# Kernel tuning notes

Measured on AMD Instinct MI355X. Metric: run time of the kernel, lower is better.

Reference implementation:

```python
import jax, jax.numpy as jnp
import numpy as np


def _layernorm(x, g, b, eps=1e-5):
    mu = jnp.mean(x, axis=-1, keepdims=True)
    var = jnp.var(x, axis=-1, keepdims=True)
    return (x - mu) * jax.lax.rsqrt(var + eps) * g + b


def _forward(x_real, x_imag, dt, conv_w, conv_b, spec_re, spec_im, lam_re, lam_im,
             dt_param, sigma, noise_r, noise_i, ln_g, ln_b, W1, b1, w2, b2,
             Jg_W, Jg_b, Rg_W, Rg_b):
    B, T, C, H, W = x_real.shape
    x = x_real + 1j * x_imag  # complex field [B,T,C,H,W]

    # ---- spatial mixer: 3x3 conv applied to real/imag parts (linear op) ----
    def conv(z):
        z2 = z.reshape(B * T, C, H, W)
        y = jax.lax.conv_general_dilated(z2, conv_w, (1, 1), 'SAME',
                                         dimension_numbers=('NCHW', 'OIHW', 'NCHW'))
        return (y + conv_b[None, :, None, None]).reshape(B, T, C, H, W)
    x = x + (conv(x.real) + 1j * conv(x.imag))

    # ---- spectral mixer: pointwise complex filter in FFT domain ----
    Xf = jnp.fft.fft2(x, axes=(-2, -1), norm='ortho')
    filt = (spec_re + 1j * spec_im)[None, None]  # [1,1,C,H,W]
    x = x + jnp.fft.ifft2(Xf * filt, axes=(-2, -1), norm='ortho')

    # ---- metriplectic propagator: diagonal SSM scan in rfft2 space ----
    dt_eff = dt * jax.nn.softplus(dt_param)          # [C]
    dt_scalar = dt_eff.mean()
    xs = jnp.concatenate([x.real, x.imag], axis=0)   # [2B,T,C,H,W]; B_out=2B
    u = jnp.fft.rfft2(xs, axes=(-2, -1), norm='ortho')  # [2B,T,C,H,Wf]
    lam = -jax.nn.softplus(lam_re) + 1j * lam_im     # stable poles, [C]
    A = jnp.exp(lam * dt_eff.astype(jnp.complex64))  # [C]
    A = jnp.broadcast_to(A[None, None, :, None, None], u.shape)

    def comb(e1, e2):  # first-order linear recurrence h_t = a_t h_{t-1} + u_t
        a1, u1 = e1
        a2, u2 = e2
        return (a1 * a2, a2 * u1 + u2)
    _, h = jax.lax.associative_scan(comb, (A, u), axis=1)

    xt = jnp.fft.irfft2(h, s=(H, W), axes=(-2, -1), norm='ortho')  # [2B,T,C,H,W] real
    x_temporal = xt[:B] + 1j * xt[B:]

    noise = (noise_r + 1j * noise_i) * sigma * jnp.sqrt(dt_scalar)
    x = x + x_temporal + noise

    # ---- Port-Hamiltonian layer on real||imag channel concat ----
    xp = jnp.transpose(x, (0, 1, 3, 4, 2))                  # [B,T,H,W,C]
    xc = jnp.concatenate([xp.real, xp.imag], axis=-1)       # [B,T,H,W,2C]
    D = 2 * C
    x_in = _layernorm(xc, ln_g, ln_b)
    # grads of potential H = sum(MLP(x_in)) wrt x_in
    pot = lambda z: (jax.nn.silu(z @ W1 + b1) @ w2 + b2).sum()
    grads = jax.grad(pot)(x_in)
    M = (x_in @ Jg_W + Jg_b).reshape(*xc.shape[:-1], D, D)
    Jm = M - jnp.swapaxes(M, -1, -2)
    P = (x_in @ Rg_W + Rg_b).reshape(*xc.shape[:-1], D, D)
    R = jnp.einsum('...ki,...kj->...ij', P, P) + 1e-4 * jnp.eye(D, dtype=xc.dtype)
    update = jnp.einsum('...ij,...j->...i', Jm - R, grads)
    x_ph = xc + update * dt_scalar

    # output: [B,T,2C,H,W]; real half = out.real, imag half = out.imag
    return jnp.transpose(x_ph, (0, 1, 4, 2, 3))


def setup_inputs() -> dict:
    key = jax.random.key(0)
    ks = jax.random.split(key, 16)
    B, T, C, H, W = 2, 8, 16, 64, 64
    D = 2 * C
    hid = D * 4
    f32 = jnp.float32
    rn = lambda k, s, sc=1.0: jax.random.normal(k, s, f32) * sc
    return dict(
        x_real=rn(ks[0], (B, T, C, H, W)),
        x_imag=rn(ks[1], (B, T, C, H, W)),
        dt=jnp.asarray(0.1, f32),
        conv_w=rn(ks[2], (C, C, 3, 3), 0.05),
        conv_b=jnp.zeros((C,), f32),
        spec_re=rn(ks[3], (C, H, W), 0.1),
        spec_im=rn(ks[4], (C, H, W), 0.1),
        lam_re=rn(ks[5], (C,)),
        lam_im=rn(ks[6], (C,)),
        dt_param=rn(ks[7], (C,)),
        sigma=jnp.asarray(0.01, f32),
        noise_r=rn(ks[8], (B, T, C, H, W)),
        noise_i=rn(ks[9], (B, T, C, H, W)),
        ln_g=jnp.ones((D,), f32),
        ln_b=jnp.zeros((D,), f32),
        W1=rn(ks[10], (D, hid), 0.1),
        b1=jnp.zeros((hid,), f32),
        w2=rn(ks[11], (hid,), 0.1),
        b2=jnp.asarray(0.0, f32),
        Jg_W=rn(ks[12], (D, D * D), 0.02),
        Jg_b=jnp.zeros((D * D,), f32),
        Rg_W=rn(ks[13], (D, D * D), 0.02),
        Rg_b=jnp.zeros((D * D,), f32),
    )


def reference(x_real, x_imag, dt, conv_w, conv_b, spec_re, spec_im, lam_re, lam_im,
              dt_param, sigma, noise_r, noise_i, ln_g, ln_b, W1, b1, w2, b2,
              Jg_W, Jg_b, Rg_W, Rg_b):
    return _forward(x_real, x_imag, dt, conv_w, conv_b, spec_re, spec_im, lam_re,
                    lam_im, dt_param, sigma, noise_r, noise_i, ln_g, ln_b, W1, b1,
                    w2, b2, Jg_W, Jg_b, Rg_W, Rg_b)
```

## Files before the change

kernel.cpp:

```cpp
#include <hip/hip_runtime.h>
#include <math.h>

#define Bb 2
#define Tt 8
#define Cc 16
#define Hh 64
#define Ww 64
#define Dd 32
#define HID 128
#define NPIX 4096
#define NIMG 256

typedef unsigned short ushort_t;
typedef unsigned int uint_t;
typedef __attribute__((ext_vector_type(8))) short short8;
typedef __attribute__((ext_vector_type(4))) float f32x4;
union U16 { uint4 u; short8 s; };

__device__ __forceinline__ float sp_f(float x) {
    return (x > 20.f) ? x : log1pf(expf(x));
}

__device__ __forceinline__ ushort_t f2bf(float f) {
    uint_t u = __float_as_uint(f);
    uint_t r = (u + 0x7fffu + ((u >> 16) & 1u)) >> 16;
    return (ushort_t)r;
}
__device__ __forceinline__ float bf2f(ushort_t h) { return __uint_as_float(((uint_t)h) << 16); }

__device__ __forceinline__ uint_t packbf(float hi, float lo) {
    return __builtin_amdgcn_perm(__float_as_uint(hi), __float_as_uint(lo), 0x07060302u);
}
__device__ __forceinline__ uint4 synth8(const float* gf, float xs) {
    uint4 r;
    r.x = packbf(gf[1] * xs, gf[0] * xs);
    r.y = packbf(gf[3] * xs, gf[2] * xs);
    r.z = packbf(gf[5] * xs, gf[4] * xs);
    r.w = packbf(gf[7] * xs, gf[6] * xs);
    return r;
}
__device__ __forceinline__ void expand8(uint4 v, float* f) {
    f[0] = __uint_as_float(v.x << 16); f[1] = __uint_as_float(v.x & 0xffff0000u);
    f[2] = __uint_as_float(v.y << 16); f[3] = __uint_as_float(v.y & 0xffff0000u);
    f[4] = __uint_as_float(v.z << 16); f[5] = __uint_as_float(v.z & 0xffff0000u);
    f[6] = __uint_as_float(v.w << 16); f[7] = __uint_as_float(v.w & 0xffff0000u);
}

typedef __attribute__((address_space(1))) const void cgvoid;
typedef __attribute__((address_space(3))) void svoid;
__device__ __forceinline__ void gload_lds16(const void* g, void* l) {
    __builtin_amdgcn_global_load_lds((cgvoid*)g, (svoid*)l, 16, 0, 0);
}

#define MFMA16(a, b, c) __builtin_amdgcn_mfma_f32_16x16x32_bf16((a), (b), (c), 0, 0, 0)

struct cpx { float r, i; };
__device__ __forceinline__ cpx cadd(cpx a, cpx b) { return {a.r + b.r, a.i + b.i}; }
__device__ __forceinline__ cpx csub(cpx a, cpx b) { return {a.r - b.r, a.i - b.i}; }
__device__ __forceinline__ cpx cmulw(cpx a, float wr, float wi) {
    return {a.r * wr - a.i * wi, a.r * wi + a.i * wr};
}
template<int S>
__device__ __forceinline__ cpx cmulSi(cpx a) {
    return {-(float)S * a.i, (float)S * a.r};
}
template<int S>
__device__ __forceinline__ void dft8(cpx* y) {
    const float C = 0.70710678118654752f;
    cpx t0 = cadd(y[0], y[4]), t1 = csub(y[0], y[4]);
    cpx t2 = cadd(y[2], y[6]), t3 = csub(y[2], y[6]);
    cpx e0 = cadd(t0, t2), e2 = csub(t0, t2);
    cpx t3i = cmulSi<S>(t3);
    cpx e1 = cadd(t1, t3i), e3 = csub(t1, t3i);
    cpx u0 = cadd(y[1], y[5]), u1 = csub(y[1], y[5]);
    cpx u2 = cadd(y[3], y[7]), u3 = csub(y[3], y[7]);
    cpx o0 = cadd(u0, u2), o2 = csub(u0, u2);
    cpx u3i = cmulSi<S>(u3);
    cpx o1 = cadd(u1, u3i), o3 = csub(u1, u3i);
    o1 = cmulw(o1, C, (float)S * C);
    o2 = cmulSi<S>(o2);
    o3 = cmulw(o3, -C, (float)S * C);
    y[0] = cadd(e0, o0); y[4] = csub(e0, o0);
    y[1] = cadd(e1, o1); y[5] = csub(e1, o1);
    y[2] = cadd(e2, o2); y[6] = csub(e2, o2);
    y[3] = cadd(e3, o3); y[7] = csub(e3, o3);
}

template<int S>
__device__ __forceinline__ void fft2d_r8(float* reM, float* imM,
                                         const float* twr, const float* twi, int tid) {
    int j = tid & 63, q = tid >> 6;
    #pragma unroll
    for (int nn = 0; nn < 2; ++nn) {
        int n2 = q * 2 + nn;
        cpx y[8];
        #pragma unroll
        for (int n1 = 0; n1 < 8; ++n1) {
            int a = j * 65 + n1 * 8 + n2;
            y[n1] = {reM[a], imM[a]};
        }
        dft8<S>(y);
        #pragma unroll
        for (int k1 = 0; k1 < 8; ++k1) {
            int m = (n2 * k1) & 63;
            cpx b = cmulw(y[k1], twr[m], twi[m]);
            int a = j * 65 + k1 * 8 + n2;
            reM[a] = b.r; imM[a] = b.i;
        }
    }
    __syncthreads();
    cpx yb[2][8];
    #pragma unroll
    for (int kk = 0; kk < 2; ++kk) {
        int k1 = q * 2 + kk;
        #pragma unroll
        for (int n2 = 0; n2 < 8; ++n2) {
            int a = j * 65 + k1 * 8 + n2;
            yb[kk][n2] = {reM[a], imM[a]};
        }
        dft8<S>(yb[kk]);
    }
    __syncthreads();
    #pragma unroll
    for (int kk = 0; kk < 2; ++kk) {
        int k1 = q * 2 + kk;
        #pragma unroll
        for (int k2 = 0; k2 < 8; ++k2) {
            int a = j * 65 + k1 + k2 * 8;
            reM[a] = yb[kk][k2].r; imM[a] = yb[kk][k2].i;
        }
    }
    __syncthreads();
    #pragma unroll
    for (int nn = 0; nn < 2; ++nn) {
        int n2 = q * 2 + nn;
        cpx y[8];
        #pragma unroll
        for (int n1 = 0; n1 < 8; ++n1) {
            int a = (n1 * 8 + n2) * 65 + j;
            y[n1] = {reM[a], imM[a]};
        }
        dft8<S>(y);
        #pragma unroll
        for (int k1 = 0; k1 < 8; ++k1) {
            int m = (n2 * k1) & 63;
            cpx b = cmulw(y[k1], twr[m], twi[m]);
            int a = (k1 * 8 + n2) * 65 + j;
            reM[a] = b.r; imM[a] = b.i;
        }
    }
    __syncthreads();
    #pragma unroll
    for (int kk = 0; kk < 2; ++kk) {
        int k1 = q * 2 + kk;
        #pragma unroll
        for (int n2 = 0; n2 < 8; ++n2) {
            int a = (k1 * 8 + n2) * 65 + j;
            yb[kk][n2] = {reM[a], imM[a]};
        }
        dft8<S>(yb[kk]);
    }
    __syncthreads();
    #pragma unroll
    for (int kk = 0; kk < 2; ++kk) {
        int k1 = q * 2 + kk;
        #pragma unroll
        for (int k2 = 0; k2 < 8; ++k2) {
            int a = (k1 + k2 * 8) * 65 + j;
            reM[a] = yb[kk][k2].r; imM[a] = yb[kk][k2].i;
        }
    }
    __syncthreads();
}

__global__ __launch_bounds__(256)
void k_conv(const float* __restrict__ xr, const float* __restrict__ xi,
            const float* __restrict__ cw, const float* __restrict__ cb,
            float2* __restrict__ x1,
            const float* __restrict__ JW, const float* __restrict__ Jb,
            const float* __restrict__ RW, const float* __restrict__ Rb,
            const float* __restrict__ W1, const float* __restrict__ dtp,
            const float* __restrict__ dt_param,
            ushort_t* __restrict__ B1t, ushort_t* __restrict__ B2t,
            ushort_t* __restrict__ w1n, ushort_t* __restrict__ w1t,
            float* __restrict__ dts_out) {
    __shared__ float sre[Cc][18][18];
    __shared__ float sim[Cc][18][18];
    __shared__ float swt[8 * 16 * 12];
    __shared__ float sb[8];
    int tid = threadIdx.x;
    if (blockIdx.x >= 512) {
        const int N1 = 96 * 1152, N2 = 32 * 1152, N3 = 4096;
        int i = (blockIdx.x - 512) * 256 + tid;
        for (; i < N1 + N2 + N3; i += 40 * 256) {
            if (i < N1) {
                int n = i / 1152, k = i % 1152;
                float v = 0.f;
                if (k < 1024) {
                    int d = k >> 5, r = k & 31;
                    if (n < 32)      v = JW[d * 1024 + n * 32 + r];
                    else if (n < 64) v = JW[d * 1024 + r * 32 + (n - 32)];
                    else             v = RW[d * 1024 + (n - 64) * 32 + r];
                } else if (k < 1056) {
                    int r = k - 1024;
                    if (n < 32)      v = Jb[n * 32 + r];
                    else if (n < 64) v = Jb[r * 32 + (n - 32)];
                    else             v = Rb[(n - 64) * 32 + r];
                }
                B1t[i] = f2bf(v);
            } else if (i < N1 + N2) {
                int i2 = i - N1;
                int n = i2 / 1152, k = i2 % 1152;
                float v = 0.f;
                if (k < 1024) {
                    int d = k >> 5, kk = k & 31;
                    v = RW[d * 1024 + kk * 32 + n];
                } else if (k < 1056) {
                    v = Rb[(k - 1024) * 32 + n];
                }
                B2t[i2] = f2bf(v);
            } else {
                int i3 = i - N1 - N2;
                int d = i3 >> 7, h = i3 & 127;
                ushort_t v = f2bf(W1[i3]);
                w1n[i3] = v;
                w1t[h * 32 + d] = v;
            }
        }
        if (blockIdx.x == 512 && tid == 0) {
            float s = 0.f;
            for (int c = 0; c < Cc; ++c) s += sp_f(dt_param[c]);
            dts_out[0] = dtp[0] * s * (1.f / Cc);
        }
        return;
    }
    int blk = blockIdx.x;
    int bt = blk >> 5;
    int sub = blk & 31;
    int tile = sub >> 1, cohalf = sub & 1;
    int ty0 = (tile >> 2) * 16, tx0 = (tile & 3) * 16;
    for (int i = tid; i < 8 * 16 * 9; i += 256) {
        int g = i / 9, k = i % 9;
        swt[g * 12 + k] = cw[cohalf * 8 * 144 + i];
    }
    if (tid < 8) sb[tid] = cb[cohalf * 8 + tid];
    for (int i = tid; i < Cc * 18 * 18; i += 256) {
        int ci = i / 324; int r = i % 324; int y = r / 18, x = r % 18;
        int gy = ty0 + y - 1, gx = tx0 + x - 1;
        float vr = 0.f, vi = 0.f;
        if (gy >= 0 && gy < Hh && gx >= 0 && gx < Ww) {
            int gidx = (bt * Cc + ci) * NPIX + gy * Ww + gx;
            vr = xr[gidx]; vi = xi[gidx];
        }
        sre[ci][y][x] = vr; sim[ci][y][x] = vi;
    }
    __syncthreads();
    int py = tid >> 4, px = tid & 15;
    int gy = ty0 + py, gx = tx0 + px;
    float ar[8], ai[8];
    #pragma unroll
    for (int oc = 0; oc < 8; ++oc) {
        int cg = cohalf * 8 + oc;
        ar[oc] = sre[cg][py + 1][px + 1] + sb[oc];
        ai[oc] = sim[cg][py + 1][px + 1] + sb[oc];
    }
    for (int ci = 0; ci < Cc; ++ci) {
        float nr[9], ni[9];
        #pragma unroll
        for (int dy = 0; dy < 3; ++dy)
            #pragma unroll
            for (int dx = 0; dx < 3; ++dx) {
                nr[dy * 3 + dx] = sre[ci][py + dy][px + dx];
                ni[dy * 3 + dx] = sim[ci][py + dy][px + dx];
            }
        #pragma unroll
        for (int oc = 0; oc < 8; ++oc) {
            const float* wp = &swt[(oc * 16 + ci) * 12];
            float4 w0 = *(const float4*)&wp[0];
            float4 w1 = *(const float4*)&wp[4];
            float w8 = wp[8];
            ar[oc] += w0.x * nr[0] + w0.y * nr[1] + w0.z * nr[2]
                    + w0.w * nr[3] + w1.x * nr[4] + w1.y * nr[5]
                    + w1.z * nr[6] + w1.w * nr[7] + w8 * nr[8];
            ai[oc] += w0.x * ni[0] + w0.y * ni[1] + w0.z * ni[2]
                    + w0.w * ni[3] + w1.x * ni[4] + w1.y * ni[5]
                    + w1.z * ni[6] + w1.w * ni[7] + w8 * ni[8];
        }
    }
    #pragma unroll
    for (int oc = 0; oc < 8; ++oc)
        x1[(bt * Cc + cohalf * 8 + oc) * NPIX + gy * Ww + gx] = make_float2(ar[oc], ai[oc]);
}

__global__ __launch_bounds__(256)
void k_fft_fwd(const float2* __restrict__ x1,
               const float* __restrict__ spec_re, const float* __restrict__ spec_im,
               float2* __restrict__ X2f) {
    int img = blockIdx.x;
    int c = img % Cc;
    int tid = threadIdx.x;
    __shared__ float re[64 * 65], im[64 * 65];
    __shared__ float twr[64], twi[64];
    if (tid < 64) {
        float ang = -0.098174770424681038798f * (float)tid;
        twr[tid] = cosf(ang); twi[tid] = sinf(ang);
    }
    const float2* src = x1 + (size_t)img * NPIX;
    for (int idx = tid; idx < NPIX; idx += 256) {
        int h = idx >> 6, w = idx & 63;
        float2 v = src[idx];
        re[h * 65 + w] = v.x; im[h * 65 + w] = v.y;
    }
    __syncthreads();
    fft2d_r8<-1>(re, im, twr, twi, tid);
    const float* fr = spec_re + c * NPIX;
    const float* fi = spec_im + c * NPIX;
    float2* dst = X2f + (size_t)img * NPIX;
    for (int idx = tid; idx < NPIX; idx += 256) {
        int h = idx >> 6, w = idx & 63;
        float xr_ = re[h * 65 + w], xi_ = im[h * 65 + w];
        float gr = 1.f + fr[idx], gi = fi[idx];
        dst[idx] = make_float2(xr_ * gr - xi_ * gi, xi_ * gr + xr_ * gi);
    }
}

__global__ __launch_bounds__(256)
void k_scan2(const float2* __restrict__ Z,
             const float* __restrict__ lam_re, const float* __restrict__ lam_im,
             const float* __restrict__ dt_param, const float* __restrict__ dtp,
             float2* __restrict__ S) {
    int id = blockIdx.x * 256 + threadIdx.x;
    int w = id & 63;
    int c = (id >> 12) & 15;
    int b = id >> 16;
    float dte = dtp[0] * sp_f(dt_param[c]);
    float ea = expf(-sp_f(lam_re[c]) * dte);
    float ph = lam_im[c] * dte;
    float Ar = ea * cosf(ph), Ai = ea * sinf(ph);
    if (w > 32) Ai = -Ai;
    bool sc = (w == 0) || (w == 32);
    int pix = id & (NPIX - 1);
    int base = (b * Tt * Cc + c) * NPIX + pix;
    float s1r = 0.f, s1i = 0.f, s2r = 0.f, s2i = 0.f;
    #pragma unroll
    for (int t = 0; t < Tt; ++t) {
        int idx = base + t * (Cc * NPIX);
        float2 zv = Z[idx];
        float nr = Ar * s1r - Ai * s1i + zv.x;
        float ni = Ar * s1i + Ai * s1r + zv.y;
        s1r = nr; s1i = ni;
        float zr, zi;
        if (sc) {
            nr = Ar * s2r + Ai * s2i + zv.x;
            ni = Ar * s2i - Ai * s2r + zv.y;
            s2r = nr; s2i = ni;
            zr = 0.5f * (s1r + s2r); zi = 0.5f * (s1i + s2i);
        } else { zr = s1r; zi = s1i; }
        S[idx] = make_float2(zv.x + zr, zv.y + zi);
    }
}

__global__ __launch_bounds__(256)
void k_fft_inv(const float2* __restrict__ Sp,
               const float* __restrict__ noise_r, const float* __restrict__ noise_i,
               const float* __restrict__ sigma_p, const float* __restrict__ dts_p,
               float2* __restrict__ xf) {
    int img = blockIdx.x; int tid = threadIdx.x;
    __shared__ float re[64 * 65], im[64 * 65];
    __shared__ float twr[64], twi[64];
    if (tid < 64) {
        float ang = 0.098174770424681038798f * (float)tid;
        twr[tid] = cosf(ang); twi[tid] = sinf(ang);
    }
    const float2* src = Sp + (size_t)img * NPIX;
    for (int idx = tid; idx < NPIX; idx += 256) {
        int h = idx >> 6, w = idx & 63;
        float2 v = src[idx];
        re[h * 65 + w] = v.x; im[h * 65 + w] = v.y;
    }
    __syncthreads();
    fft2d_r8<1>(re, im, twr, twi, tid);
    float ns = sigma_p[0] * sqrtf(dts_p[0]);
    const float inv = 1.f / 4096.f;
    float2* dst = xf + (size_t)img * NPIX;
    const float* nr = noise_r + (size_t)img * NPIX;
    const float* ni = noise_i + (size_t)img * NPIX;
    for (int idx = tid; idx < NPIX; idx += 256) {
        int h = idx >> 6, w = idx & 63;
        dst[idx] = make_float2(re[h * 65 + w] * inv + ns * nr[idx],
                               im[h * 65 + w] * inv + ns * ni[idx]);
    }
}

__global__ __launch_bounds__(256, 2)
void k_ph(const float2* __restrict__ field,
          const float* __restrict__ ln_g, const float* __restrict__ ln_b,
          const float* __restrict__ b1, const float* __restrict__ w2,
          const ushort_t* __restrict__ w1n, const ushort_t* __restrict__ w1t,
          const ushort_t* __restrict__ B1t, const ushort_t* __restrict__ B2t,
          const float* __restrict__ dts_p,
          float* __restrict__ out) {
    __shared__ ushort_t xin_s[128 * 40];
    __shared__ ushort_t g_s[128 * 40];
    __shared__ ushort_t pg_s[128 * 40];
    __shared__ ushort_t A_s[128 * 136];

    int tid = threadIdx.x;
    int bt = blockIdx.x >> 5;
    int pix0 = (blockIdx.x & 31) << 7;

    int p = tid & 127, half = tid >> 7;
    const float2* fbase = field + ((size_t)bt * 16) * NPIX + pix0 + p;
    float2 xv[8];
    float s1 = 0.f, s2 = 0.f;
    #pragma unroll
    for (int j = 0; j < 8; ++j) {
        xv[j] = fbase[(half * 8 + j) * NPIX];
        s1 += xv[j].x + xv[j].y;
        s2 += xv[j].x * xv[j].x + xv[j].y * xv[j].y;
    }
    float2* red = (float2*)A_s;
    red[p * 2 + half] = make_float2(s1, s2);
    __syncthreads();
    float2 r0 = red[p * 2], r1 = red[p * 2 + 1];
    float mu = (r0.x + r1.x) * 0.03125f;
    float var = (r0.y + r1.y) * 0.03125f - mu * mu;
    float rs = rsqrtf(var + 1e-5f);
    #pragma unroll
    for (int j = 0; j < 8; ++j) {
        int cf = half * 8 + j;
        xin_s[p * 40 + cf]      = f2bf((xv[j].x - mu) * rs * ln_g[cf] + ln_b[cf]);
        xin_s[p * 40 + cf + 16] = f2bf((xv[j].y - mu) * rs * ln_g[cf + 16] + ln_b[cf + 16]);
    }
    __syncthreads();

    int lane = tid & 63, wv = tid >> 6;
    int quad = lane >> 4, l15 = lane & 15;
    const f32x4 zero4 = {0.f, 0.f, 0.f, 0.f};

    int m0z = wv * 32;
    f32x4 zacc[2][8];
    #pragma unroll
    for (int mt = 0; mt < 2; ++mt)
        #pragma unroll
        for (int nt = 0; nt < 8; ++nt) zacc[mt][nt] = zero4;
    U16 az[2];
    #pragma unroll
    for (int mt = 0; mt < 2; ++mt)
        az[mt].u = *(const uint4*)&xin_s[(m0z + mt * 16 + l15) * 40 + quad * 8];
    #pragma unroll
    for (int nt = 0; nt < 8; ++nt) {
        U16 bz;
        bz.u = *(const uint4*)&w1t[(nt * 16 + l15) * 32 + quad * 8];
        zacc[0][nt] = MFMA16(az[0].s, bz.s, zacc[0][nt]);
        zacc[1][nt] = MFMA16(az[1].s, bz.s, zacc[1][nt]);
    }
    #pragma unroll
    for (int nt = 0; nt < 8; ++nt) {
        int col = nt * 16 + l15;
        float b1v = b1[col], w2v = w2[col];
        #pragma unroll
        for (int mt = 0; mt < 2; ++mt) {
            #pragma unroll
            for (int r = 0; r < 4; ++r) {
                int row = m0z + mt * 16 + quad * 4 + r;
                float z = zacc[mt][nt][r] + b1v;
                float s = 1.f / (1.f + expf(-z));
                float t = s * (1.f + z * (1.f - s)) * w2v;
                A_s[row * 136 + col] = f2bf(t);
            }
        }
    }

    f32x4 gacc[2][2];
    #pragma unroll
    for (int mt = 0; mt < 2; ++mt)
        #pragma unroll
        for (int nt = 0; nt < 2; ++nt) gacc[mt][nt] = zero4;
    #pragma unroll
    for (int q = 0; q < 4; ++q) {
        U16 ag[2];
        #pragma unroll
        for (int mt = 0; mt < 2; ++mt)
            ag[mt].u = *(const uint4*)&A_s[(m0z + mt * 16 + l15) * 136 + q * 32 + quad * 8];
        #pragma unroll
        for (int nt = 0; nt < 2; ++nt) {
            U16 bg;
            bg.u = *(const uint4*)&w1n[(nt * 16 + l15) * 128 + q * 32 + quad * 8];
            gacc[0][nt] = MFMA16(ag[0].s, bg.s, gacc[0][nt]);
            gacc[1][nt] = MFMA16(ag[1].s, bg.s, gacc[1][nt]);
        }
    }
    #pragma unroll
    for (int mt = 0; mt < 2; ++mt)
        #pragma unroll
        for (int nt = 0; nt < 2; ++nt)
            #pragma unroll
            for (int r = 0; r < 4; ++r)
                g_s[(m0z + mt * 16 + quad * 4 + r) * 40 + nt * 16 + l15] = f2bf(gacc[mt][nt][r]);
    __syncthreads();

    int mh = wv & 1, nh = wv >> 1;
    ushort_t* stage = A_s;
    uint_t xw[4][16];
    uint4 gvp[4];
    float gf[4][8];
    #pragma unroll
    for (int mt = 0; mt < 4; ++mt) {
        int row = mh * 64 + mt * 16 + l15;
        #pragma unroll
        for (int q = 0; q < 4; ++q)
            *(uint4*)&xw[mt][q * 4] = *(const uint4*)&xin_s[row * 40 + q * 8];
        gvp[mt] = *(const uint4*)&g_s[row * 40 + quad * 8];
        expand8(gvp[mt], gf[mt]);
    }

    {
        const ushort_t* gp;
        if (wv == 0) {
            gp = B1t + (0 * 16 + (lane & 15)) * 1152 + (lane >> 4) * 8;
            gload_lds16(gp, stage + 0 * 512);
            gp = B1t + (4 * 16 + (lane & 15)) * 1152 + (lane >> 4) * 8;
            gload_lds16(gp, stage + 4 * 512);
        } else if (wv == 1) {
            gp = B1t + (1 * 16 + (lane & 15)) * 1152 + (lane >> 4) * 8;
            gload_lds16(gp, stage + 1 * 512);
            gp = B1t + (5 * 16 + (lane & 15)) * 1152 + (lane >> 4) * 8;
            gload_lds16(gp, stage + 5 * 512);
        } else if (wv == 2) {
            gp = B1t + (2 * 16 + (lane & 15)) * 1152 + (lane >> 4) * 8;
            gload_lds16(gp, stage + 2 * 512);
        } else {
            gp = B1t + (3 * 16 + (lane & 15)) * 1152 + (lane >> 4) * 8;
            gload_lds16(gp, stage + 3 * 512);
        }
    }
    f32x4 acc1[3][4];
    #pragma unroll
    for (int j = 0; j < 3; ++j)
        #pragma unroll
        for (int mt = 0; mt < 4; ++mt) acc1[j][mt] = zero4;
    #pragma unroll
    for (int s = 0; s < 33; ++s) {
        __syncthreads();
        int par = s & 1;
        if (s < 32) {
            int sn = s + 1, pn = sn & 1;
            const ushort_t* gp;
            if (wv == 0) {
                gp = B1t + (0 * 16 + (lane & 15)) * 1152 + sn * 32 + (lane >> 4) * 8;
                gload_lds16(gp, stage + pn * 3072 + 0 * 512);
                gp = B1t + (4 * 16 + (lane & 15)) * 1152 + sn * 32 + (lane >> 4) * 8;
                gload_lds16(gp, stage + pn * 3072 + 4 * 512);
            } else if (wv == 1) {
                gp = B1t + (1 * 16 + (lane & 15)) * 1152 + sn * 32 + (lane >> 4) * 8;
                gload_lds16(gp, stage + pn * 3072 + 1 * 512);
                gp = B1t + (5 * 16 + (lane & 15)) * 1152 + sn * 32 + (lane >> 4) * 8;
                gload_lds16(gp, stage + pn * 3072 + 5 * 512);
            } else if (wv == 2) {
                gp = B1t + (2 * 16 + (lane & 15)) * 1152 + sn * 32 + (lane >> 4) * 8;
                gload_lds16(gp, stage + pn * 3072 + 2 * 512);
            } else {
                gp = B1t + (3 * 16 + (lane & 15)) * 1152 + sn * 32 + (lane >> 4) * 8;
                gload_lds16(gp, stage + pn * 3072 + 3 * 512);
            }
        }
        U16 bfr[3];
        #pragma unroll
        for (int j = 0; j < 3; ++j)
            bfr[j].u = *(const uint4*)&stage[par * 3072 + (nh + 2 * j) * 512 + lane * 8];
        #pragma unroll
        for (int mt = 0; mt < 4; ++mt) {
            U16 a;
            if (s < 32) {
                uint_t u = xw[mt][s >> 1];
                float xs = (s & 1) ? __uint_as_float(u & 0xffff0000u)
                                   : __uint_as_float(u << 16);
                a.u = synth8(gf[mt], xs);
            } else {
                a.u = gvp[mt];
            }
            #pragma unroll
            for (int j = 0; j < 3; ++j)
                acc1[j][mt] = MFMA16(a.s, bfr[j].s, acc1[j][mt]);
        }
    }
    f32x4 um[4];
    #pragma unroll
    for (int mt = 0; mt < 4; ++mt) {
        um[mt] = acc1[0][mt] - acc1[1][mt];
        #pragma unroll
        for (int r = 0; r < 4; ++r)
            pg_s[(mh * 64 + mt * 16 + quad * 4 + r) * 40 + nh * 16 + l15] = f2bf(acc1[2][mt][r]);
    }
    __syncthreads();

    uint4 pgp[4];
    float pgf[4][8];
    #pragma unroll
    for (int mt = 0; mt < 4; ++mt) {
        int row = mh * 64 + mt * 16 + l15;
        pgp[mt] = *(const uint4*)&pg_s[row * 40 + quad * 8];
        expand8(pgp[mt], pgf[mt]);
    }
    {
        if (wv == 2) {
            const ushort_t* gp = B2t + (0 * 16 + (lane & 15)) * 1152 + (lane >> 4) * 8;
            gload_lds16(gp, stage + 0 * 512);
        } else if (wv == 3) {
            const ushort_t* gp = B2t + (1 * 16 + (lane & 15)) * 1152 + (lane >> 4) * 8;
            gload_lds16(gp, stage + 1 * 512);
        }
    }
    f32x4 acc2[4];
    #pragma unroll
    for (int mt = 0; mt < 4; ++mt) acc2[mt] = zero4;
    #pragma unroll
    for (int s = 0; s < 33; ++s) {
        __syncthreads();
        int par = s & 1;
        if (s < 32) {
            int sn = s + 1, pn = sn & 1;
            if (wv == 2) {
                const ushort_t* gp = B2t + (0 * 16 + (lane & 15)) * 1152 + sn * 32 + (lane >> 4) * 8;
                gload_lds16(gp, stage + pn * 3072 + 0 * 512);
            } else if (wv == 3) {
                const ushort_t* gp = B2t + (1 * 16 + (lane & 15)) * 1152 + sn * 32 + (lane >> 4) * 8;
                gload_lds16(gp, stage + pn * 3072 + 1 * 512);
            }
        }
        U16 bfr;
        bfr.u = *(const uint4*)&stage[par * 3072 + nh * 512 + lane * 8];
        #pragma unroll
        for (int mt = 0; mt < 4; ++mt) {
            U16 a;
            if (s < 32) {
                uint_t u = xw[mt][s >> 1];
                float xs = (s & 1) ? __uint_as_float(u & 0xffff0000u)
                                   : __uint_as_float(u << 16);
                a.u = synth8(pgf[mt], xs);
            } else {
                a.u = pgp[mt];
            }
            acc2[mt] = MFMA16(a.s, bfr.s, acc2[mt]);
        }
    }

    __syncthreads();
    float* upd = (float*)&A_s[8192];
    #pragma unroll
    for (int mt = 0; mt < 4; ++mt) {
        int col = nh * 16 + l15;
        #pragma unroll
        for (int r = 0; r < 4; ++r) {
            int row = mh * 64 + mt * 16 + quad * 4 + r;
            float gval = bf2f(g_s[row * 40 + col]);
            upd[row * 33 + col] = um[mt][r] - acc2[mt][r] - 1e-4f * gval;
        }
    }
    __syncthreads();
    float dts = dts_p[0];
    #pragma unroll
    for (int cc = 0; cc < 16; ++cc) {
        int c = half * 16 + cc;
        float2 v = fbase[cc * NPIX];
        float xcv = half ? v.y : v.x;
        out[((size_t)bt * 32 + c) * NPIX + pix0 + p] = xcv + dts * upd[p * 33 + c];
    }
}

extern "C" void kernel_launch(void* const* d_in, const int* in_sizes, int n_in,
                              void* d_out, int out_size, void* d_ws, size_t ws_size,
                              hipStream_t stream) {
    const float* x_real   = (const float*)d_in[0];
    const float* x_imag   = (const float*)d_in[1];
    const float* dt       = (const float*)d_in[2];
    const float* conv_w   = (const float*)d_in[3];
    const float* conv_b   = (const float*)d_in[4];
    const float* spec_re  = (const float*)d_in[5];
    const float* spec_im  = (const float*)d_in[6];
    const float* lam_re   = (const float*)d_in[7];
    const float* lam_im   = (const float*)d_in[8];
    const float* dt_param = (const float*)d_in[9];
    const float* sigma    = (const float*)d_in[10];
    const float* noise_r  = (const float*)d_in[11];
    const float* noise_i  = (const float*)d_in[12];
    const float* ln_g     = (const float*)d_in[13];
    const float* ln_b     = (const float*)d_in[14];
    const float* W1       = (const float*)d_in[15];
    const float* b1       = (const float*)d_in[16];
    const float* w2       = (const float*)d_in[17];
    const float* Jg_W     = (const float*)d_in[19];
    const float* Jg_b     = (const float*)d_in[20];
    const float* Rg_W     = (const float*)d_in[21];
    const float* Rg_b     = (const float*)d_in[22];

    float2* wsA = (float2*)d_ws;
    float2* wsB = wsA + 1048576;
    float2* wsS = wsB + 1048576;

    ushort_t* B1t = (ushort_t*)(wsS + 1048576);
    ushort_t* B2t = B1t + 96 * 1152;
    ushort_t* w1n = B2t + 32 * 1152;
    ushort_t* w1t = w1n + 4096;
    float*    dts = (float*)(w1t + 4096);

    k_conv<<<552, 256, 0, stream>>>(x_real, x_imag, conv_w, conv_b, wsA,
                                    Jg_W, Jg_b, Rg_W, Rg_b, W1, dt, dt_param,
                                    B1t, B2t, w1n, w1t, dts);
    k_fft_fwd<<<NIMG, 256, 0, stream>>>(wsA, spec_re, spec_im, wsB);
    k_scan2<<<512, 256, 0, stream>>>(wsB, lam_re, lam_im, dt_param, dt, wsS);
    k_fft_inv<<<NIMG, 256, 0, stream>>>(wsS, noise_r, noise_i, sigma, dts, wsA);
    k_ph<<<512, 256, 0, stream>>>(wsA, ln_g, ln_b, b1, w2, w1n, w1t, B1t, B2t, dts,
                                  (float*)d_out);
}
```

Measured before the change: 213.7 us.

## Pre-swizzle PH weights into fragment order and double FFT block threads

The Port-Hamiltonian GEMM weights are now written by the prep kernel directly in per-lane MFMA fragment order. Each wave loads its B fragments straight from global memory into registers with a two-deep prefetch, replacing the LDS staging through global_load_lds and the per-step __syncthreads. Separately, the FFT kernels move from 256 to 512 threads so each thread handles one radix-8 column group instead of two, which lowers register pressure and raises parallelism per image. The trade-off is more redundant global/L2 traffic per wave and higher register use for the prefetched fragments.

```diff
diff --git a/kernel.cpp b/kernel.cpp
--- a/kernel.cpp
+++ b/kernel.cpp
@@ -44,12 +44,6 @@
     f[2] = __uint_as_float(v.y << 16); f[3] = __uint_as_float(v.y & 0xffff0000u);
     f[4] = __uint_as_float(v.z << 16); f[5] = __uint_as_float(v.z & 0xffff0000u);
     f[6] = __uint_as_float(v.w << 16); f[7] = __uint_as_float(v.w & 0xffff0000u);
-}
-
-typedef __attribute__((address_space(1))) const void cgvoid;
-typedef __attribute__((address_space(3))) void svoid;
-__device__ __forceinline__ void gload_lds16(const void* g, void* l) {
-    __builtin_amdgcn_global_load_lds((cgvoid*)g, (svoid*)l, 16, 0, 0);
 }
 
 #define MFMA16(a, b, c) __builtin_amdgcn_mfma_f32_16x16x32_bf16((a), (b), (c), 0, 0, 0)
@@ -89,85 +83,70 @@
 template<int S>
 __device__ __forceinline__ void fft2d_r8(float* reM, float* imM,
                                          const float* twr, const float* twi, int tid) {
-    int j = tid & 63, q = tid >> 6;
-    #pragma unroll
-    for (int nn = 0; nn < 2; ++nn) {
-        int n2 = q * 2 + nn;
+    int j = tid & 63, g = tid >> 6;
+    {
         cpx y[8];
         #pragma unroll
         for (int n1 = 0; n1 < 8; ++n1) {
-            int a = j * 65 + n1 * 8 + n2;
+            int a = j * 65 + n1 * 8 + g;
             y[n1] = {reM[a], imM[a]};
         }
         dft8<S>(y);
         #pragma unroll
         for (int k1 = 0; k1 < 8; ++k1) {
-            int m = (n2 * k1) & 63;
+            int m = (g * k1) & 63;
             cpx b = cmulw(y[k1], twr[m], twi[m]);
-            int a = j * 65 + k1 * 8 + n2;
+            int a = j * 65 + k1 * 8 + g;
             reM[a] = b.r; imM[a] = b.i;
         }
     }
     __syncthreads();
-    cpx yb[2][8];
-    #pragma unroll
-    for (int kk = 0; kk < 2; ++kk) {
-        int k1 = q * 2 + kk;
+    {
+        cpx y[8];
         #pragma unroll
         for (int n2 = 0; n2 < 8; ++n2) {
-            int a = j * 65 + k1 * 8 + n2;
-            yb[kk][n2] = {reM[a], imM[a]};
-        }
-        dft8<S>(yb[kk]);
-    }
-    __syncthreads();
-    #pragma unroll
-    for (int kk = 0; kk < 2; ++kk) {
-        int k1 = q * 2 + kk;
+            int a = j * 65 + g * 8 + n2;
+            y[n2] = {reM[a], imM[a]};
+        }
+        dft8<S>(y);
+        __syncthreads();
         #pragma unroll
         for (int k2 = 0; k2 < 8; ++k2) {
-            int a = j * 65 + k1 + k2 * 8;
-            reM[a] = yb[kk][k2].r; imM[a] = yb[kk][k2].i;
-        }
-    }
-    __syncthreads();
-    #pragma unroll
-    for (int nn = 0; nn < 2; ++nn) {
-        int n2 = q * 2 + nn;
+            int a = j * 65 + g + k2 * 8;
+            reM[a] = y[k2].r; imM[a] = y[k2].i;
+        }
+    }
+    __syncthreads();
+    {
         cpx y[8];
         #pragma unroll
         for (int n1 = 0; n1 < 8; ++n1) {
-            int a = (n1 * 8 + n2) * 65 + j;
+            int a = (n1 * 8 + g) * 65 + j;
             y[n1] = {reM[a], imM[a]};
         }
         dft8<S>(y);
         #pragma unroll
         for (int k1 = 0; k1 < 8; ++k1) {
-            int m = (n2 * k1) & 63;
+            int m = (g * k1) & 63;
             cpx b = cmulw(y[k1], twr[m], twi[m]);
-            int a = (k1 * 8 + n2) * 65 + j;
+            int a = (k1 * 8 + g) * 65 + j;
             reM[a] = b.r; imM[a] = b.i;
         }
     }
     __syncthreads();
-    #pragma unroll
-    for (int kk = 0; kk < 2; ++kk) {
-        int k1 = q * 2 + kk;
+    {
+        cpx y[8];
         #pragma unroll
         for (int n2 = 0; n2 < 8; ++n2) {
-            int a = (k1 * 8 + n2) * 65 + j;
-            yb[kk][n2] = {reM[a], imM[a]};
-        }
-        dft8<S>(yb[kk]);
-    }
-    __syncthreads();
-    #pragma unroll
-    for (int kk = 0; kk < 2; ++kk) {
-        int k1 = q * 2 + kk;
+            int a = (g * 8 + n2) * 65 + j;
+            y[n2] = {reM[a], imM[a]};
+        }
+        dft8<S>(y);
+        __syncthreads();
         #pragma unroll
         for (int k2 = 0; k2 < 8; ++k2) {
-            int a = (k1 + k2 * 8) * 65 + j;
-            reM[a] = yb[kk][k2].r; imM[a] = yb[kk][k2].i;
+            int a = (g + k2 * 8) * 65 + j;
+            reM[a] = y[k2].r; imM[a] = y[k2].i;
         }
     }
     __syncthreads();
@@ -181,7 +160,7 @@
             const float* __restrict__ RW, const float* __restrict__ Rb,
             const float* __restrict__ W1, const float* __restrict__ dtp,
             const float* __restrict__ dt_param,
-            ushort_t* __restrict__ B1t, ushort_t* __restrict__ B2t,
+            ushort_t* __restrict__ B1f, ushort_t* __restrict__ B2f,
             ushort_t* __restrict__ w1n, ushort_t* __restrict__ w1t,
             float* __restrict__ dts_out) {
     __shared__ float sre[Cc][18][18];
@@ -190,35 +169,41 @@
     __shared__ float sb[8];
     int tid = threadIdx.x;
     if (blockIdx.x >= 512) {
-        const int N1 = 96 * 1152, N2 = 32 * 1152, N3 = 4096;
+        const int N1 = 33 * 3072, N2 = 33 * 1024, N3 = 4096;
         int i = (blockIdx.x - 512) * 256 + tid;
         for (; i < N1 + N2 + N3; i += 40 * 256) {
             if (i < N1) {
-                int n = i / 1152, k = i % 1152;
-                float v = 0.f;
+                int s = i / 3072; int r = i % 3072;
+                int ch = r >> 9; int lane = (r >> 3) & 63; int e = i & 7;
+                int n = ch * 16 + (lane & 15);
+                int k = s * 32 + ((lane >> 4) << 3) + e;
+                float v;
                 if (k < 1024) {
-                    int d = k >> 5, r = k & 31;
-                    if (n < 32)      v = JW[d * 1024 + n * 32 + r];
-                    else if (n < 64) v = JW[d * 1024 + r * 32 + (n - 32)];
-                    else             v = RW[d * 1024 + (n - 64) * 32 + r];
-                } else if (k < 1056) {
-                    int r = k - 1024;
-                    if (n < 32)      v = Jb[n * 32 + r];
-                    else if (n < 64) v = Jb[r * 32 + (n - 32)];
-                    else             v = Rb[(n - 64) * 32 + r];
+                    int d = k >> 5, rr = k & 31;
+                    if (n < 32)      v = JW[d * 1024 + n * 32 + rr];
+                    else if (n < 64) v = JW[d * 1024 + rr * 32 + (n - 32)];
+                    else             v = RW[d * 1024 + (n - 64) * 32 + rr];
+                } else {
+                    int rr = k - 1024;
+                    if (n < 32)      v = Jb[n * 32 + rr];
+                    else if (n < 64) v = Jb[rr * 32 + (n - 32)];
+                    else             v = Rb[(n - 64) * 32 + rr];
                 }
-                B1t[i] = f2bf(v);
+                B1f[i] = f2bf(v);
             } else if (i < N1 + N2) {
                 int i2 = i - N1;
-                int n = i2 / 1152, k = i2 % 1152;
-                float v = 0.f;
+                int s = i2 / 1024; int r = i2 % 1024;
+                int ch = r >> 9; int lane = (r >> 3) & 63; int e = i2 & 7;
+                int n = ch * 16 + (lane & 15);
+                int k = s * 32 + ((lane >> 4) << 3) + e;
+                float v;
                 if (k < 1024) {
                     int d = k >> 5, kk = k & 31;
                     v = RW[d * 1024 + kk * 32 + n];
-                } else if (k < 1056) {
+                } else {
                     v = Rb[(k - 1024) * 32 + n];
                 }
-                B2t[i2] = f2bf(v);
+                B2f[i2] = f2bf(v);
             } else {
                 int i3 = i - N1 - N2;
                 int d = i3 >> 7, h = i3 & 127;
@@ -292,7 +277,7 @@
         x1[(bt * Cc + cohalf * 8 + oc) * NPIX + gy * Ww + gx] = make_float2(ar[oc], ai[oc]);
 }
 
-__global__ __launch_bounds__(256)
+__global__ __launch_bounds__(512)
 void k_fft_fwd(const float2* __restrict__ x1,
                const float* __restrict__ spec_re, const float* __restrict__ spec_im,
                float2* __restrict__ X2f) {
@@ -306,7 +291,7 @@
         twr[tid] = cosf(ang); twi[tid] = sinf(ang);
     }
     const float2* src = x1 + (size_t)img * NPIX;
-    for (int idx = tid; idx < NPIX; idx += 256) {
+    for (int idx = tid; idx < NPIX; idx += 512) {
         int h = idx >> 6, w = idx & 63;
         float2 v = src[idx];
         re[h * 65 + w] = v.x; im[h * 65 + w] = v.y;
@@ -316,7 +301,7 @@
     const float* fr = spec_re + c * NPIX;
     const float* fi = spec_im + c * NPIX;
     float2* dst = X2f + (size_t)img * NPIX;
-    for (int idx = tid; idx < NPIX; idx += 256) {
+    for (int idx = tid; idx < NPIX; idx += 512) {
         int h = idx >> 6, w = idx & 63;
         float xr_ = re[h * 65 + w], xi_ = im[h * 65 + w];
         float gr = 1.f + fr[idx], gi = fi[idx];
@@ -360,7 +345,7 @@
     }
 }
 
-__global__ __launch_bounds__(256)
+__global__ __launch_bounds__(512)
 void k_fft_inv(const float2* __restrict__ Sp,
                const float* __restrict__ noise_r, const float* __restrict__ noise_i,
                const float* __restrict__ sigma_p, const float* __restrict__ dts_p,
@@ -373,7 +358,7 @@
         twr[tid] = cosf(ang); twi[tid] = sinf(ang);
     }
     const float2* src = Sp + (size_t)img * NPIX;
-    for (int idx = tid; idx < NPIX; idx += 256) {
+    for (int idx = tid; idx < NPIX; idx += 512) {
         int h = idx >> 6, w = idx & 63;
         float2 v = src[idx];
         re[h * 65 + w] = v.x; im[h * 65 + w] = v.y;
@@ -385,7 +370,7 @@
     float2* dst = xf + (size_t)img * NPIX;
     const float* nr = noise_r + (size_t)img * NPIX;
     const float* ni = noise_i + (size_t)img * NPIX;
-    for (int idx = tid; idx < NPIX; idx += 256) {
+    for (int idx = tid; idx < NPIX; idx += 512) {
         int h = idx >> 6, w = idx & 63;
         dst[idx] = make_float2(re[h * 65 + w] * inv + ns * nr[idx],
                                im[h * 65 + w] * inv + ns * ni[idx]);
@@ -397,7 +382,7 @@
           const float* __restrict__ ln_g, const float* __restrict__ ln_b,
           const float* __restrict__ b1, const float* __restrict__ w2,
           const ushort_t* __restrict__ w1n, const ushort_t* __restrict__ w1t,
-          const ushort_t* __restrict__ B1t, const ushort_t* __restrict__ B2t,
+          const ushort_t* __restrict__ B1f, const ushort_t* __restrict__ B2f,
           const float* __restrict__ dts_p,
           float* __restrict__ out) {
     __shared__ ushort_t xin_s[128 * 40];
@@ -501,7 +486,8 @@
     __syncthreads();
 
     int mh = wv & 1, nh = wv >> 1;
-    ushort_t* stage = A_s;
+    const uint4* B1v = (const uint4*)B1f;
+    const uint4* B2v = (const uint4*)B2f;
     uint_t xw[4][16];
     uint4 gvp[4];
     float gf[4][8];
@@ -515,26 +501,12 @@
         expand8(gvp[mt], gf[mt]);
     }
 
-    {
-        const ushort_t* gp;
-        if (wv == 0) {
-            gp = B1t + (0 * 16 + (lane & 15)) * 1152 + (lane >> 4) * 8;
-            gload_lds16(gp, stage + 0 * 512);
-            gp = B1t + (4 * 16 + (lane & 15)) * 1152 + (lane >> 4) * 8;
-            gload_lds16(gp, stage + 4 * 512);
-        } else if (wv == 1) {
-            gp = B1t + (1 * 16 + (lane & 15)) * 1152 + (lane >> 4) * 8;
-            gload_lds16(gp, stage + 1 * 512);
-            gp = B1t + (5 * 16 + (lane & 15)) * 1152 + (lane >> 4) * 8;
-            gload_lds16(gp, stage + 5 * 512);
-        } else if (wv == 2) {
-            gp = B1t + (2 * 16 + (lane & 15)) * 1152 + (lane >> 4) * 8;
-            gload_lds16(gp, stage + 2 * 512);
-        } else {
-            gp = B1t + (3 * 16 + (lane & 15)) * 1152 + (lane >> 4) * 8;
-            gload_lds16(gp, stage + 3 * 512);
-        }
-    }
+    uint4 br[2][3];
+    #pragma unroll
+    for (int pf = 0; pf < 2; ++pf)
+        #pragma unroll
+        for (int jj = 0; jj < 3; ++jj)
+            br[pf][jj] = B1v[(pf * 6 + nh + 2 * jj) * 64 + lane];
     f32x4 acc1[3][4];
     #pragma unroll
     for (int j = 0; j < 3; ++j)
@@ -542,33 +514,9 @@
         for (int mt = 0; mt < 4; ++mt) acc1[j][mt] = zero4;
     #pragma unroll
     for (int s = 0; s < 33; ++s) {
-        __syncthreads();
-        int par = s & 1;
-        if (s < 32) {
-            int sn = s + 1, pn = sn & 1;
-            const ushort_t* gp;
-            if (wv == 0) {
-                gp = B1t + (0 * 16 + (lane & 15)) * 1152 + sn * 32 + (lane >> 4) * 8;
-                gload_lds16(gp, stage + pn * 3072 + 0 * 512);
-                gp = B1t + (4 * 16 + (lane & 15)) * 1152 + sn * 32 + (lane >> 4) * 8;
-                gload_lds16(gp, stage + pn * 3072 + 4 * 512);
-            } else if (wv == 1) {
-                gp = B1t + (1 * 16 + (lane & 15)) * 1152 + sn * 32 + (lane >> 4) * 8;
-                gload_lds16(gp, stage + pn * 3072 + 1 * 512);
-                gp = B1t + (5 * 16 + (lane & 15)) * 1152 + sn * 32 + (lane >> 4) * 8;
-                gload_lds16(gp, stage + pn * 3072 + 5 * 512);
-            } else if (wv == 2) {
-                gp = B1t + (2 * 16 + (lane & 15)) * 1152 + sn * 32 + (lane >> 4) * 8;
-                gload_lds16(gp, stage + pn * 3072 + 2 * 512);
-            } else {
-                gp = B1t + (3 * 16 + (lane & 15)) * 1152 + sn * 32 + (lane >> 4) * 8;
-                gload_lds16(gp, stage + pn * 3072 + 3 * 512);
-            }
-        }
-        U16 bfr[3];
-        #pragma unroll
-        for (int j = 0; j < 3; ++j)
-            bfr[j].u = *(const uint4*)&stage[par * 3072 + (nh + 2 * j) * 512 + lane * 8];
+        int cur = s & 1;
+        U16 b3[3];
+        b3[0].u = br[cur][0]; b3[1].u = br[cur][1]; b3[2].u = br[cur][2];
         #pragma unroll
         for (int mt = 0; mt < 4; ++mt) {
             U16 a;
@@ -580,9 +528,14 @@
             } else {
                 a.u = gvp[mt];
             }
+            acc1[0][mt] = MFMA16(a.s, b3[0].s, acc1[0][mt]);
+            acc1[1][mt] = MFMA16(a.s, b3[1].s, acc1[1][mt]);
+            acc1[2][mt] = MFMA16(a.s, b3[2].s, acc1[2][mt]);
+        }
+        if (s + 2 < 33) {
             #pragma unroll
-            for (int j = 0; j < 3; ++j)
-                acc1[j][mt] = MFMA16(a.s, bfr[j].s, acc1[j][mt]);
+            for (int jj = 0; jj < 3; ++jj)
+                br[cur][jj] = B1v[((s + 2) * 6 + nh + 2 * jj) * 64 + lane];
         }
     }
     f32x4 um[4];
@@ -603,34 +556,17 @@
         pgp[mt] = *(const uint4*)&pg_s[row * 40 + quad * 8];
         expand8(pgp[mt], pgf[mt]);
     }
-    {
-        if (wv == 2) {
-            const ushort_t* gp = B2t + (0 * 16 + (lane & 15)) * 1152 + (lane >> 4) * 8;
-            gload_lds16(gp, stage + 0 * 512);
-        } else if (wv == 3) {
-            const ushort_t* gp = B2t + (1 * 16 + (lane & 15)) * 1152 + (lane >> 4) * 8;
-            gload_lds16(gp, stage + 1 * 512);
-        }
-    }
+    uint4 br2[2];
+    br2[0] = B2v[(0 * 2 + nh) * 64 + lane];
+    br2[1] = B2v[(1 * 2 + nh) * 64 + lane];
     f32x4 acc2[4];
     #pragma unroll
     for (int mt = 0; mt < 4; ++mt) acc2[mt] = zero4;
     #pragma unroll
     for (int s = 0; s < 33; ++s) {
-        __syncthreads();
-        int par = s & 1;
-        if (s < 32) {
-            int sn = s + 1, pn = sn & 1;
-            if (wv == 2) {
-                const ushort_t* gp = B2t + (0 * 16 + (lane & 15)) * 1152 + sn * 32 + (lane >> 4) * 8;
-                gload_lds16(gp, stage + pn * 3072 + 0 * 512);
-            } else if (wv == 3) {
-                const ushort_t* gp = B2t + (1 * 16 + (lane & 15)) * 1152 + sn * 32 + (lane >> 4) * 8;
-                gload_lds16(gp, stage + pn * 3072 + 1 * 512);
-            }
-        }
-        U16 bfr;
-        bfr.u = *(const uint4*)&stage[par * 3072 + nh * 512 + lane * 8];
+        int cur = s & 1;
+        U16 b;
+        b.u = br2[cur];
         #pragma unroll
         for (int mt = 0; mt < 4; ++mt) {
             U16 a;
@@ -642,8 +578,10 @@
             } else {
                 a.u = pgp[mt];
             }
-            acc2[mt] = MFMA16(a.s, bfr.s, acc2[mt]);
-        }
+            acc2[mt] = MFMA16(a.s, b.s, acc2[mt]);
+        }
+        if (s + 2 < 33)
+            br2[cur] = B2v[((s + 2) * 2 + nh) * 64 + lane];
     }
 
     __syncthreads();
@@ -699,18 +637,18 @@
     float2* wsB = wsA + 1048576;
     float2* wsS = wsB + 1048576;
 
-    ushort_t* B1t = (ushort_t*)(wsS + 1048576);
-    ushort_t* B2t = B1t + 96 * 1152;
-    ushort_t* w1n = B2t + 32 * 1152;
+    ushort_t* B1f = (ushort_t*)(wsS + 1048576);
+    ushort_t* B2f = B1f + 33 * 3072;
+    ushort_t* w1n = B2f + 33 * 1024;
     ushort_t* w1t = w1n + 4096;
     float*    dts = (float*)(w1t + 4096);
 
     k_conv<<<552, 256, 0, stream>>>(x_real, x_imag, conv_w, conv_b, wsA,
                                     Jg_W, Jg_b, Rg_W, Rg_b, W1, dt, dt_param,
-                                    B1t, B2t, w1n, w1t, dts);
-    k_fft_fwd<<<NIMG, 256, 0, stream>>>(wsA, spec_re, spec_im, wsB);
+                                    B1f, B2f, w1n, w1t, dts);
+    k_fft_fwd<<<NIMG, 512, 0, stream>>>(wsA, spec_re, spec_im, wsB);
     k_scan2<<<512, 256, 0, stream>>>(wsB, lam_re, lam_im, dt_param, dt, wsS);
-    k_fft_inv<<<NIMG, 256, 0, stream>>>(wsS, noise_r, noise_i, sigma, dts, wsA);
-    k_ph<<<512, 256, 0, stream>>>(wsA, ln_g, ln_b, b1, w2, w1n, w1t, B1t, B2t, dts,
+    k_fft_inv<<<NIMG, 512, 0, stream>>>(wsS, noise_r, noise_i, sigma, dts, wsA);
+    k_ph<<<512, 256, 0, stream>>>(wsA, ln_g, ln_b, b1, w2, w1n, w1t, B1f, B2f, dts,
                                   (float*)d_out);
 }
```

After: 201.0 us. 1.06x faster.
